# Optimization experiments

Hardware: AMD Instinct MI355X
Metric: run time of the kernel (lower is better)

## Reference

```python
import jax, jax.numpy as jnp
import numpy as np

B, NV, NRINGS, NDIRS, C, F = 2, 20000, 8, 8, 16, 16


def setup_inputs() -> dict:
    key = jax.random.key(0)
    ks = jax.random.split(key, 7)
    y = jax.random.normal(ks[0], (B, NV, NDIRS, C), jnp.float32)
    contributors = jax.random.randint(ks[1], (NV, NRINGS, NDIRS, 3), 0, NV, dtype=jnp.int32)
    weights_bary = jax.random.uniform(ks[2], (NV, NRINGS, NDIRS, 3), jnp.float32)
    angles = jax.random.randint(ks[3], (NV, NRINGS, NDIRS, 3), 0, NDIRS, dtype=jnp.int32)
    kernel = jax.random.normal(ks[4], (NRINGS, NDIRS, C, F), jnp.float32) * 0.05
    center_kernel = jax.random.normal(ks[5], (C, F), jnp.float32) * 0.05
    bias = jnp.zeros((F,), jnp.float32)
    return {"y": y, "contributors": contributors, "weights_bary": weights_bary,
            "angles": angles, "kernel": kernel, "center_kernel": center_kernel, "bias": bias}


def reference(y, contributors, weights_bary, angles, kernel, center_kernel, bias):
    # y: (B, nv, ndirs, C); tables: (nv, nrings, ndirs, 3)
    b, nv, ndirs, nch = y.shape
    nfilters = kernel.shape[-1]
    nrings = contributors.shape[1]

    # window_interpolation_sync: gather 3 contributor vertices per window bin,
    # with the direction axis re-indexed per-contributor (radial sync), then
    # barycentric-weighted sum.  Flatten (vertex, dir) into one gather index.
    idx = contributors * ndirs + angles                 # (nv, nrings, ndirs, 3)
    y_flat = y.reshape(b, nv * ndirs, nch)
    gathered = y_flat[:, idx, :]                        # (B, nv, nrings, ndirs, 3, C)
    z = jnp.einsum('bvrdjc,vrdj->bvrdc', gathered, weights_bary)  # (B, nv, nrings, ndirs, C)

    # gcnn_conv: circular pad over dirs then VALID conv with (nrings, ndirs) kernel
    zr = z.reshape(b * nv, nrings, ndirs, nch)
    zr = jnp.concatenate([zr, zr[:, :, :-1, :]], axis=2)  # width 2*ndirs-1
    conv = jax.lax.conv_general_dilated(
        zr, kernel, window_strides=(1, 1), padding='VALID',
        dimension_numbers=('NHWC', 'HWIO', 'NHWC'))       # (B*nv, 1, ndirs, F)
    conv = conv.reshape(b, nv, ndirs, nfilters)

    out = conv + jnp.einsum('bvdc,cf->bvdf', y, center_kernel) + bias
    out = jax.nn.relu(out)
    return jnp.max(out, axis=2)                          # take_max over directions -> (B, nv, F)
```

## Files before the change

kernel.cpp:

```cpp
#include <hip/hip_runtime.h>

typedef unsigned short u16;
typedef __attribute__((ext_vector_type(4))) unsigned int u32x4;
typedef __attribute__((ext_vector_type(4))) float f32x4;
typedef __attribute__((ext_vector_type(8))) __bf16 bf16x8;

constexpr int BATCH = 2;
constexpr int NV    = 20000;
constexpr int ND    = 8;
constexpr int CH    = 16;
constexpr int NF    = 16;
constexpr int NVD   = NV * ND;
constexpr int NCHUNK = 36;
constexpr int MTOT  = BATCH * NV;
constexpr int BSTR  = 40;

constexpr size_t Y16_OFF_B = 0;
constexpr size_t K2C_OFF_B = 10240000;

__device__ __forceinline__ u16 f2bf(float x) {
    unsigned int u = __float_as_uint(x);
    unsigned int r = (u + 0x7fffu + ((u >> 16) & 1u)) >> 16;
    return (u16)r;
}
__device__ __forceinline__ unsigned int pack2bf(float a, float b) {
    return (unsigned int)f2bf(a) | ((unsigned int)f2bf(b) << 16);
}

__global__ __launch_bounds__(256) void prep(const float* __restrict__ y,
                                            u16* __restrict__ y16) {
    int tid = blockIdx.x * 256 + threadIdx.x;
    const float4* src = (const float4*)(y + (size_t)tid * 16);
    float4 v0 = src[0], v1 = src[1], v2 = src[2], v3 = src[3];
    u32x4 lo = {pack2bf(v0.x, v0.y), pack2bf(v0.z, v0.w), pack2bf(v1.x, v1.y), pack2bf(v1.z, v1.w)};
    u32x4 hi = {pack2bf(v2.x, v2.y), pack2bf(v2.z, v2.w), pack2bf(v3.x, v3.y), pack2bf(v3.z, v3.w)};
    u16* yd = y16 + (size_t)tid * 16;
    *(u32x4*)(yd)     = lo;
    *(u32x4*)(yd + 8) = hi;
}

__global__ __launch_bounds__(256) void k2_build(const float* __restrict__ kern,
                                                const float* __restrict__ ck,
                                                u16* __restrict__ k2c) {
    int e = blockIdx.x * 256 + threadIdx.x;
    int i = e & 4095;
    int kc = e >> 12;
    int n = i >> 5, kk = i & 31;
    int k = kc * 32 + kk;
    int w = n >> 4, f = n & 15;
    float val;
    if (k < 1024) {
        int r = k >> 7, dd = (k >> 4) & 7, c = k & 15;
        int d = (dd - w) & 7;
        val = kern[((r * 8 + d) * 16 + c) * 16 + f];
    } else {
        int ke = k - 1024;
        int d = ke >> 4, c = ke & 15;
        val = (d == w) ? ck[c * 16 + f] : 0.f;
    }
    k2c[e] = f2bf(val);
}

__global__ __launch_bounds__(256) void fused_gather_gemm(const u16* __restrict__ y16,
                                                         const int* __restrict__ contrib,
                                                         const float* __restrict__ wbary,
                                                         const int* __restrict__ angles,
                                                         const u16* __restrict__ k2c,
                                                         const float* __restrict__ bias,
                                                         float* __restrict__ out) {
    __shared__ __align__(16) u16 Bb[2][128 * BSTR];
    const int t = threadIdx.x;
    const int w = t >> 6, lane = t & 63;
    const int lrow = lane & 15, lq = lane >> 4;
    const int s_p = lq >> 1;
    const int h8  = (lq & 1) * 8;
    const int m0 = blockIdx.x * 64;
    const int arow = m0 + w * 16 + lrow;
    const int b_p = (arow >= NV);
    const int v_p = arow - b_p * NV;
    const u16* __restrict__ yb = y16 + (size_t)b_p * NVD * CH + h8;
    const int mb0 = v_p * 192 + s_p * 3;
    const int sn = t >> 1, sh = (t & 1) * 16;

    int   ce0, ce1, ce2, ae0, ae1, ae2;  float we0, we1, we2;
    int   co0, co1, co2, ao0, ao1, ao2;  float wo0, wo1, wo2;
    u32x4 ge0, ge1, ge2;  float ve0, ve1, ve2;
    u32x4 go0, go1, go2;  float vo0, vo1, vo2;
    u32x4 bne0, bne1, bno0, bno1;

    f32x4 acc[8];
    #pragma unroll
    for (int nt = 0; nt < 8; ++nt) acc[nt] = (f32x4){0.f, 0.f, 0.f, 0.f};

#define META_ISSUE(S, KC_) { const int o_ = mb0 + (KC_) * 6;                       \
    c##S##0 = contrib[o_]; c##S##1 = contrib[o_ + 1]; c##S##2 = contrib[o_ + 2];   \
    a##S##0 = angles[o_];  a##S##1 = angles[o_ + 1];  a##S##2 = angles[o_ + 2];    \
    w##S##0 = wbary[o_];   w##S##1 = wbary[o_ + 1];   w##S##2 = wbary[o_ + 2]; }

#define G_ISSUE(S, KC_) {                                                          \
    if ((KC_) < 32) {                                                              \
        g##S##0 = *(const u32x4*)(yb + (size_t)((unsigned)c##S##0 * 128u +         \
                                                (unsigned)a##S##0 * 16u));         \
        g##S##1 = *(const u32x4*)(yb + (size_t)((unsigned)c##S##1 * 128u +         \
                                                (unsigned)a##S##1 * 16u));         \
        g##S##2 = *(const u32x4*)(yb + (size_t)((unsigned)c##S##2 * 128u +         \
                                                (unsigned)a##S##2 * 16u));         \
        v##S##0 = w##S##0; v##S##1 = w##S##1; v##S##2 = w##S##2;                   \
    } else {                                                                       \
        g##S##0 = *(const u32x4*)(yb + (size_t)((unsigned)v_p * 128u +             \
                                      (unsigned)(2 * ((KC_) - 32) + s_p) * 16u));  \
    } }

#define COMBINE(S, KC_, A_) {                                                      \
    if ((KC_) < 32) {                                                              \
        float ac_[8];                                                              \
        _Pragma("unroll") for (int x_ = 0; x_ < 8; ++x_) ac_[x_] = 0.f;            \
        _Pragma("unroll")                                                          \
        for (int q_ = 0; q_ < 4; ++q_) {                                           \
            unsigned u0_ = g##S##0[q_], u1_ = g##S##1[q_], u2_ = g##S##2[q_];      \
            ac_[2 * q_]     += v##S##0 * __uint_as_float(u0_ << 16);               \
            ac_[2 * q_ + 1] += v##S##0 * __uint_as_float(u0_ & 0xffff0000u);       \
            ac_[2 * q_]     += v##S##1 * __uint_as_float(u1_ << 16);               \
            ac_[2 * q_ + 1] += v##S##1 * __uint_as_float(u1_ & 0xffff0000u);       \
            ac_[2 * q_]     += v##S##2 * __uint_as_float(u2_ << 16);               \
            ac_[2 * q_ + 1] += v##S##2 * __uint_as_float(u2_ & 0xffff0000u);       \
        }                                                                          \
        u32x4 o_;                                                                  \
        _Pragma("unroll") for (int q_ = 0; q_ < 4; ++q_)                           \
            o_[q_] = pack2bf(ac_[2 * q_], ac_[2 * q_ + 1]);                        \
        A_ = *(bf16x8*)&o_;                                                        \
    } else { u32x4 o_ = g##S##0; A_ = *(bf16x8*)&o_; } }

    META_ISSUE(e, 0); META_ISSUE(o, 1);
    {
        const u32x4* src = (const u32x4*)(k2c + (size_t)0 * 4096 + sn * 32 + sh);
        u32x4 b0 = src[0], b1 = src[1];
        u16* dst = &Bb[0][sn * BSTR + sh];
        *(u32x4*)(dst)     = b0;
        *(u32x4*)(dst + 8) = b1;
    }
    G_ISSUE(e, 0); META_ISSUE(e, 2);
    G_ISSUE(o, 1);
    {
        const u32x4* src = (const u32x4*)(k2c + (size_t)1 * 4096 + sn * 32 + sh);
        bno0 = src[0]; bno1 = src[1];
    }

    for (int p = 0; p < 18; ++p) {
        const int k0 = 2 * p, k1 = 2 * p + 1;

        __syncthreads();
        if (k0 + 2 < NCHUNK) {
            const u32x4* src = (const u32x4*)(k2c + (size_t)(k0 + 2) * 4096 + sn * 32 + sh);
            bne0 = src[0]; bne1 = src[1];
        }
        bf16x8 aev;
        COMBINE(e, k0, aev);
        if (k0 + 2 < NCHUNK) G_ISSUE(e, k0 + 2);
        if (k0 + 3 < 32)     META_ISSUE(o, k0 + 3);
        {
            bf16x8 bf[8];
            #pragma unroll
            for (int nt = 0; nt < 8; ++nt)
                bf[nt] = *(const bf16x8*)(&Bb[0][(nt * 16 + lrow) * BSTR + lq * 8]);
            #pragma unroll
            for (int nt = 0; nt < 8; ++nt)
                acc[nt] = __builtin_amdgcn_mfma_f32_16x16x32_bf16(aev, bf[nt], acc[nt], 0, 0, 0);
        }
        {
            u16* dst = &Bb[1][sn * BSTR + sh];
            *(u32x4*)(dst)     = bno0;
            *(u32x4*)(dst + 8) = bno1;
        }

        __syncthreads();
        if (k1 + 2 < NCHUNK) {
            const u32x4* src = (const u32x4*)(k2c + (size_t)(k1 + 2) * 4096 + sn * 32 + sh);
            bno0 = src[0]; bno1 = src[1];
        }
        bf16x8 aov;
        COMBINE(o, k1, aov);
        if (k1 + 2 < NCHUNK) G_ISSUE(o, k1 + 2);
        if (k1 + 3 < 32)     META_ISSUE(e, k1 + 3);
        {
            bf16x8 bf[8];
            #pragma unroll
            for (int nt = 0; nt < 8; ++nt)
                bf[nt] = *(const bf16x8*)(&Bb[1][(nt * 16 + lrow) * BSTR + lq * 8]);
            #pragma unroll
            for (int nt = 0; nt < 8; ++nt)
                acc[nt] = __builtin_amdgcn_mfma_f32_16x16x32_bf16(aov, bf[nt], acc[nt], 0, 0, 0);
        }
        if (k1 + 1 < NCHUNK) {
            u16* dst = &Bb[0][sn * BSTR + sh];
            *(u32x4*)(dst)     = bne0;
            *(u32x4*)(dst + 8) = bne1;
        }
    }
#undef META_ISSUE
#undef G_ISSUE
#undef COMBINE

    const float bb = bias[lrow];
    #pragma unroll
    for (int reg = 0; reg < 4; ++reg) {
        float m = 0.f;
        #pragma unroll
        for (int nt = 0; nt < 8; ++nt) m = fmaxf(m, acc[nt][reg] + bb);
        out[((size_t)(m0 + w * 16 + lq * 4 + reg)) * NF + lrow] = m;
    }
}

extern "C" void kernel_launch(void* const* d_in, const int* in_sizes, int n_in,
                              void* d_out, int out_size, void* d_ws, size_t ws_size,
                              hipStream_t stream) {
    const float* y      = (const float*)d_in[0];
    const int*   contrib= (const int*)d_in[1];
    const float* wbary  = (const float*)d_in[2];
    const int*   angles = (const int*)d_in[3];
    const float* kern   = (const float*)d_in[4];
    const float* ck     = (const float*)d_in[5];
    const float* bias   = (const float*)d_in[6];
    float* out = (float*)d_out;

    u16* y16 = (u16*)((char*)d_ws + Y16_OFF_B);
    u16* k2c = (u16*)((char*)d_ws + K2C_OFF_B);

    prep<<<1250, 256, 0, stream>>>(y, y16);
    k2_build<<<(NCHUNK * 4096) / 256, 256, 0, stream>>>(kern, ck, k2c);
    fused_gather_gemm<<<MTOT / 64, 256, 0, stream>>>(y16, contrib, wbary, angles,
                                                     k2c, bias, out);
}
```

Measured before the change: 239.5 us.

## Split GEMM K dimension across two blocks and reduce partials in separate kernel

The fused gather-GEMM grid is doubled, and each block now handles half of the 36 K-chunks for its 64 rows. Each half writes its full 128-column partial accumulator to a workspace buffer. A new combine_max kernel sums the two partials, adds bias and takes the relu/max over directions. The aim is more parallelism and latency hiding from twice as many blocks. The cost is a large partial-sum round trip through global memory (two halves × 128 × 40000 floats), an extra launch, and duplicated per-block prologue work.

```diff
diff --git a/kernel.cpp b/kernel.cpp
--- a/kernel.cpp
+++ b/kernel.cpp
@@ -14,9 +14,11 @@
 constexpr int NCHUNK = 36;
 constexpr int MTOT  = BATCH * NV;
 constexpr int BSTR  = 40;
+constexpr int KSPLIT_CH = 18;
 
 constexpr size_t Y16_OFF_B = 0;
 constexpr size_t K2C_OFF_B = 10240000;
+constexpr size_t PB_OFF_B  = 10534912;
 
 __device__ __forceinline__ u16 f2bf(float x) {
     unsigned int u = __float_as_uint(x);
@@ -66,15 +68,17 @@
                                                          const float* __restrict__ wbary,
                                                          const int* __restrict__ angles,
                                                          const u16* __restrict__ k2c,
-                                                         const float* __restrict__ bias,
-                                                         float* __restrict__ out) {
+                                                         float* __restrict__ pb) {
     __shared__ __align__(16) u16 Bb[2][128 * BSTR];
     const int t = threadIdx.x;
+    const int s  = blockIdx.x & 1;
+    const int kcBeg = s * KSPLIT_CH;
+    const int kcEnd = kcBeg + KSPLIT_CH;
     const int w = t >> 6, lane = t & 63;
     const int lrow = lane & 15, lq = lane >> 4;
     const int s_p = lq >> 1;
     const int h8  = (lq & 1) * 8;
-    const int m0 = blockIdx.x * 64;
+    const int m0 = (blockIdx.x >> 1) * 64;
     const int arow = m0 + w * 16 + lrow;
     const int b_p = (arow >= NV);
     const int v_p = arow - b_p * NV;
@@ -131,33 +135,33 @@
         A_ = *(bf16x8*)&o_;                                                        \
     } else { u32x4 o_ = g##S##0; A_ = *(bf16x8*)&o_; } }
 
-    META_ISSUE(e, 0); META_ISSUE(o, 1);
+    META_ISSUE(e, kcBeg); META_ISSUE(o, kcBeg + 1);
     {
-        const u32x4* src = (const u32x4*)(k2c + (size_t)0 * 4096 + sn * 32 + sh);
+        const u32x4* src = (const u32x4*)(k2c + (size_t)kcBeg * 4096 + sn * 32 + sh);
         u32x4 b0 = src[0], b1 = src[1];
         u16* dst = &Bb[0][sn * BSTR + sh];
         *(u32x4*)(dst)     = b0;
         *(u32x4*)(dst + 8) = b1;
     }
-    G_ISSUE(e, 0); META_ISSUE(e, 2);
-    G_ISSUE(o, 1);
+    G_ISSUE(e, kcBeg); META_ISSUE(e, kcBeg + 2);
+    G_ISSUE(o, kcBeg + 1);
     {
-        const u32x4* src = (const u32x4*)(k2c + (size_t)1 * 4096 + sn * 32 + sh);
+        const u32x4* src = (const u32x4*)(k2c + (size_t)(kcBeg + 1) * 4096 + sn * 32 + sh);
         bno0 = src[0]; bno1 = src[1];
     }
 
-    for (int p = 0; p < 18; ++p) {
-        const int k0 = 2 * p, k1 = 2 * p + 1;
+    for (int p = 0; p < KSPLIT_CH / 2; ++p) {
+        const int k0 = kcBeg + 2 * p, k1 = k0 + 1;
 
         __syncthreads();
-        if (k0 + 2 < NCHUNK) {
+        if (k0 + 2 < kcEnd) {
             const u32x4* src = (const u32x4*)(k2c + (size_t)(k0 + 2) * 4096 + sn * 32 + sh);
             bne0 = src[0]; bne1 = src[1];
         }
         bf16x8 aev;
         COMBINE(e, k0, aev);
-        if (k0 + 2 < NCHUNK) G_ISSUE(e, k0 + 2);
-        if (k0 + 3 < 32)     META_ISSUE(o, k0 + 3);
+        if (k0 + 2 < kcEnd) G_ISSUE(e, k0 + 2);
+        if (k0 + 3 < kcEnd && k0 + 3 < 32) META_ISSUE(o, k0 + 3);
         {
             bf16x8 bf[8];
             #pragma unroll
@@ -174,14 +178,14 @@
         }
 
         __syncthreads();
-        if (k1 + 2 < NCHUNK) {
+        if (k1 + 2 < kcEnd) {
             const u32x4* src = (const u32x4*)(k2c + (size_t)(k1 + 2) * 4096 + sn * 32 + sh);
             bno0 = src[0]; bno1 = src[1];
         }
         bf16x8 aov;
         COMBINE(o, k1, aov);
-        if (k1 + 2 < NCHUNK) G_ISSUE(o, k1 + 2);
-        if (k1 + 3 < 32)     META_ISSUE(e, k1 + 3);
+        if (k1 + 2 < kcEnd) G_ISSUE(o, k1 + 2);
+        if (k1 + 3 < kcEnd && k1 + 3 < 32) META_ISSUE(e, k1 + 3);
         {
             bf16x8 bf[8];
             #pragma unroll
@@ -191,7 +195,7 @@
             for (int nt = 0; nt < 8; ++nt)
                 acc[nt] = __builtin_amdgcn_mfma_f32_16x16x32_bf16(aov, bf[nt], acc[nt], 0, 0, 0);
         }
-        if (k1 + 1 < NCHUNK) {
+        if (k1 + 1 < kcEnd) {
             u16* dst = &Bb[0][sn * BSTR + sh];
             *(u32x4*)(dst)     = bne0;
             *(u32x4*)(dst + 8) = bne1;
@@ -201,14 +205,38 @@
 #undef G_ISSUE
 #undef COMBINE
 
-    const float bb = bias[lrow];
-    #pragma unroll
-    for (int reg = 0; reg < 4; ++reg) {
-        float m = 0.f;
+    float* pbs = pb + (size_t)(s * 128) * MTOT;
+    #pragma unroll
+    for (int nt = 0; nt < 8; ++nt) {
+        *(f32x4*)(pbs + (size_t)(nt * 16 + lrow) * MTOT + m0 + w * 16 + lq * 4) = acc[nt];
+    }
+}
+
+__global__ __launch_bounds__(256) void combine_max(const float* __restrict__ pb,
+                                                   const float* __restrict__ bias,
+                                                   float* __restrict__ out) {
+    int tid = blockIdx.x * 256 + threadIdx.x;
+    if (tid >= 2 * MTOT) return;
+    int row = tid >> 1, half = tid & 1;
+    const float* p0 = pb + row;
+    const float* p1 = pb + (size_t)128 * MTOT + row;
+    float bs[8], m[8];
+    #pragma unroll
+    for (int j = 0; j < 8; ++j) { bs[j] = bias[half * 8 + j]; m[j] = 0.f; }
+    #pragma unroll
+    for (int w = 0; w < 8; ++w) {
         #pragma unroll
-        for (int nt = 0; nt < 8; ++nt) m = fmaxf(m, acc[nt][reg] + bb);
-        out[((size_t)(m0 + w * 16 + lq * 4 + reg)) * NF + lrow] = m;
-    }
+        for (int j = 0; j < 8; ++j) {
+            int n = w * 16 + half * 8 + j;
+            float v = p0[(size_t)n * MTOT] + p1[(size_t)n * MTOT] + bs[j];
+            m[j] = fmaxf(m[j], v);
+        }
+    }
+    float4 o0 = {m[0], m[1], m[2], m[3]};
+    float4 o1 = {m[4], m[5], m[6], m[7]};
+    float* dst = out + (size_t)row * NF + half * 8;
+    *(float4*)(dst)     = o0;
+    *(float4*)(dst + 4) = o1;
 }
 
 extern "C" void kernel_launch(void* const* d_in, const int* in_sizes, int n_in,
@@ -223,11 +251,13 @@
     const float* bias   = (const float*)d_in[6];
     float* out = (float*)d_out;
 
-    u16* y16 = (u16*)((char*)d_ws + Y16_OFF_B);
-    u16* k2c = (u16*)((char*)d_ws + K2C_OFF_B);
+    u16*   y16 = (u16*)((char*)d_ws + Y16_OFF_B);
+    u16*   k2c = (u16*)((char*)d_ws + K2C_OFF_B);
+    float* pb  = (float*)((char*)d_ws + PB_OFF_B);
 
     prep<<<1250, 256, 0, stream>>>(y, y16);
     k2_build<<<(NCHUNK * 4096) / 256, 256, 0, stream>>>(kern, ck, k2c);
-    fused_gather_gemm<<<MTOT / 64, 256, 0, stream>>>(y16, contrib, wbary, angles,
-                                                     k2c, bias, out);
-}
+    fused_gather_gemm<<<2 * (MTOT / 64), 256, 0, stream>>>(y16, contrib, wbary, angles,
+                                                           k2c, pb);
+    combine_max<<<(2 * MTOT + 255) / 256, 256, 0, stream>>>(pb, bias, out);
+}
```

Result: slower. 249.8 us (+4.3%).
